# Kernel optimization log

Measured on AMD Instinct MI355X. Metric: run time of the kernel, lower is better.

Reference implementation:

```python
import jax, jax.numpy as jnp
import numpy as np

N_NODES = 50000


def gcn_conv(x, W, b, src, dst, n_nodes):
    # PyG GCNConv: h = D^{-1/2} (A + I) D^{-1/2} (x W) + b
    h = x @ W  # [N, out]
    # degree with self loops: deg[i] = in_degree(i) + 1
    deg = jax.ops.segment_sum(jnp.ones_like(dst, dtype=h.dtype), dst, num_segments=n_nodes) + 1.0
    dis = jax.lax.rsqrt(deg)  # deg >= 1 always
    norm = dis[src] * dis[dst]  # [E]
    # gather-scale-scatter over edges
    agg = jax.ops.segment_sum(h[src] * norm[:, None], dst, num_segments=n_nodes)
    # self-loop contribution: norm_ii = dis[i]^2
    agg = agg + h * (dis * dis)[:, None]
    return agg + b


def setup_inputs() -> dict:
    key = jax.random.key(0)
    k1, k2, k3, k4, k5, k6 = jax.random.split(key, 6)
    latent, hidden, out = 64, 96, 64
    x = jax.random.normal(k1, (N_NODES, latent), dtype=jnp.float32)
    edge_index = jax.random.randint(k2, (2, 800000), 0, N_NODES, dtype=jnp.int64)
    W1 = jax.random.normal(k3, (latent, hidden), dtype=jnp.float32) / np.sqrt(latent)
    b1 = jnp.zeros((hidden,), dtype=jnp.float32)
    W2 = jax.random.normal(k4, (hidden, out), dtype=jnp.float32) / np.sqrt(hidden)
    b2 = jnp.zeros((out,), dtype=jnp.float32)
    return {"x": x, "edge_index": edge_index, "W1": W1, "b1": b1, "W2": W2, "b2": b2}


def reference(x, edge_index, W1, b1, W2, b2):
    src, dst = edge_index[0], edge_index[1]
    n = x.shape[0]
    h = jax.nn.relu(gcn_conv(x, W1, b1, src, dst, n))
    out = jax.nn.sigmoid(gcn_conv(h, W2, b2, src, dst, n))
    return out
```

## Files before the change

### kernel.cpp

```cpp
#include <hip/hip_runtime.h>
#include <hip/hip_bf16.h>
#include <hip/hip_fp16.h>

constexpr int G1 = 96;
constexpr int RNODES = 12544;
constexpr int CAP = 64;

__global__ __launch_bounds__(256) void histo_kernel(const int* __restrict__ dst,
                                                    unsigned short* __restrict__ hist,
                                                    int E, int chunk, int npad2) {
    __shared__ unsigned int h32[RNODES / 2];
    int g = blockIdx.x;
    int base = blockIdx.y * RNODES;
    int e0 = g * chunk;
    int e1 = min(e0 + chunk, E);
    for (int i = threadIdx.x; i < RNODES / 2; i += 256) h32[i] = 0;
    __syncthreads();
    for (int e = e0 + threadIdx.x; e < e1; e += 256) {
        int d = dst[e] - base;
        if ((unsigned)d < (unsigned)RNODES) atomicAdd(&h32[d >> 1], 1u << ((d & 1) * 16));
    }
    __syncthreads();
    for (int i = threadIdx.x; i < RNODES; i += 256)
        hist[(size_t)g * npad2 + base + i] =
            (unsigned short)((h32[i >> 1] >> ((i & 1) * 16)) & 0xFFFFu);
}

__global__ __launch_bounds__(256) void colscan_cast_kernel(
    const unsigned short* __restrict__ hist, unsigned short* __restrict__ off16,
    int* __restrict__ cnt, float* __restrict__ dis, const float* __restrict__ x,
    __half* __restrict__ Th, int N, int npad2) {
    __shared__ float sdis[256];
    int n0 = blockIdx.x * 256;
    int d = n0 + threadIdx.x;
    float dv = 0.f;
    if (d < N) {
        int run = 0;
        for (int g = 0; g < G1; ++g) {
            off16[(size_t)g * npad2 + d] = (unsigned short)run;
            run += hist[(size_t)g * npad2 + d];
        }
        cnt[d] = run;
        dv = rsqrtf((float)run + 1.0f);
        dis[d] = dv;
    }
    sdis[threadIdx.x] = dv;
    __syncthreads();
    int total = min(256, N - n0) * 64;
    size_t base_elem = (size_t)n0 * 64;
    for (int l = threadIdx.x * 8; l < total; l += 256 * 8) {
        float dn = sdis[l >> 6];
        float4 a = *(const float4*)(x + base_elem + l);
        float4 b = *(const float4*)(x + base_elem + l + 4);
        __half2 h[4];
        h[0] = __floats2half2_rn(a.x * dn, a.y * dn);
        h[1] = __floats2half2_rn(a.z * dn, a.w * dn);
        h[2] = __floats2half2_rn(b.x * dn, b.y * dn);
        h[3] = __floats2half2_rn(b.z * dn, b.w * dn);
        *(float4*)(Th + base_elem + l) = *(float4*)h;
    }
}

__global__ __launch_bounds__(256) void fill_bucket16_kernel(
    const int* __restrict__ src, const int* __restrict__ dst,
    const unsigned short* __restrict__ off16, unsigned short* __restrict__ csr16,
    int E, int chunk, int npad2) {
    __shared__ unsigned int c16[RNODES / 2];
    int g = blockIdx.x;
    int base = blockIdx.y * RNODES;
    const unsigned int* op = (const unsigned int*)(off16 + (size_t)g * npad2 + base);
    for (int i = threadIdx.x; i < RNODES / 2; i += 256) c16[i] = op[i];
    __syncthreads();
    int e0 = g * chunk;
    int e1 = min(e0 + chunk, E);
    for (int e = e0 + threadIdx.x; e < e1; e += 256) {
        int d = dst[e] - base;
        if ((unsigned)d < (unsigned)RNODES) {
            unsigned int sh = (d & 1) * 16;
            unsigned int old = atomicAdd(&c16[d >> 1], 1u << sh);
            unsigned int rank = (old >> sh) & 0xFFFFu;
            if (rank < CAP) csr16[(size_t)(base + d) * CAP + rank] = (unsigned short)src[e];
        }
    }
}

__global__ void zero_int_kernel(int* __restrict__ p, int N) {
    int i = blockIdx.x * blockDim.x + threadIdx.x;
    if (i < N) p[i] = 0;
}
__global__ void degree_int_kernel(const int* __restrict__ dst, int* __restrict__ cnt, int E) {
    int i = blockIdx.x * blockDim.x + threadIdx.x;
    if (i < E) atomicAdd(&cnt[dst[i]], 1);
}
__global__ void dis_from_cnt_kernel(const int* __restrict__ cnt, float* __restrict__ dis, int N) {
    int i = blockIdx.x * blockDim.x + threadIdx.x;
    if (i < N) dis[i] = rsqrtf((float)cnt[i] + 1.0f);
}
__global__ __launch_bounds__(1024) void scan_kernel(const int* __restrict__ cnt,
                                                    int* __restrict__ cursor, int N) {
    constexpr int T = 1024;
    __shared__ int sums[T];
    int t = threadIdx.x;
    int ch = (N + T - 1) / T;
    int base = t * ch;
    int local = 0;
    for (int k = 0; k < ch; ++k) {
        int idx = base + k;
        if (idx < N) local += cnt[idx];
    }
    sums[t] = local;
    __syncthreads();
    for (int off = 1; off < T; off <<= 1) {
        int add = (t >= off) ? sums[t - off] : 0;
        __syncthreads();
        sums[t] += add;
        __syncthreads();
    }
    int run = sums[t] - local;
    for (int k = 0; k < ch; ++k) {
        int idx = base + k;
        if (idx < N) {
            cursor[idx] = run;
            run += cnt[idx];
        }
    }
}
__global__ void fill_atomic_kernel(const int* __restrict__ src, const int* __restrict__ dst,
                                   int* __restrict__ cursor_mut, int* __restrict__ csr_src,
                                   int E) {
    int e = blockIdx.x * blockDim.x + threadIdx.x;
    if (e >= E) return;
    int pos = atomicAdd(&cursor_mut[dst[e]], 1);
    csr_src[pos] = src[e];
}
__global__ void cast_scale_kernel(const float* __restrict__ X, const float* __restrict__ dis,
                                  __half* __restrict__ Th, int N) {
    int i = blockIdx.x * blockDim.x + threadIdx.x;
    int n = i >> 3;
    if (n >= N) return;
    int c = (i & 7) * 8;
    float dn = dis[n];
    float4 a = *(const float4*)(X + (size_t)n * 64 + c);
    float4 b = *(const float4*)(X + (size_t)n * 64 + c + 4);
    __half2 h[4];
    h[0] = __floats2half2_rn(a.x * dn, a.y * dn);
    h[1] = __floats2half2_rn(a.z * dn, a.w * dn);
    h[2] = __floats2half2_rn(b.x * dn, b.y * dn);
    h[3] = __floats2half2_rn(b.z * dn, b.w * dn);
    *(float4*)(Th + (size_t)n * 64 + c) = *(float4*)h;
}

__device__ __forceinline__ void gather_batch16(const unsigned short* __restrict__ bucket,
                                               int j0, int scnt,
                                               const __half* __restrict__ Xh, int c,
                                               float a[16]) {
    uint4 raw = *(const uint4*)(bucket + j0);
    unsigned int w[4] = {raw.x, raw.y, raw.z, raw.w};
    float4 r0[8], r1[8];
#pragma unroll
    for (int k = 0; k < 8; ++k) {
        if (k < scnt) {
            int s = (w[k >> 1] >> ((k & 1) * 16)) & 0xFFFF;
            const __half* row = Xh + (size_t)s * 64 + c;
            r0[k] = *(const float4*)(row);
            r1[k] = *(const float4*)(row + 8);
        }
    }
#pragma unroll
    for (int k = 0; k < 8; ++k) {
        if (k < scnt) {
            const __half2* h0 = (const __half2*)&r0[k];
            const __half2* h1 = (const __half2*)&r1[k];
#pragma unroll
            for (int q = 0; q < 4; ++q) {
                float2 f0 = __half22float2(h0[q]);
                float2 f1 = __half22float2(h1[q]);
                a[2 * q] += f0.x;
                a[2 * q + 1] += f0.y;
                a[8 + 2 * q] += f1.x;
                a[8 + 2 * q + 1] += f1.y;
            }
        }
    }
}

__device__ __forceinline__ void add_row16(const __half* __restrict__ row, float a[16]) {
    float4 r0 = *(const float4*)(row);
    float4 r1 = *(const float4*)(row + 8);
    const __half2* h0 = (const __half2*)&r0;
    const __half2* h1 = (const __half2*)&r1;
#pragma unroll
    for (int q = 0; q < 4; ++q) {
        float2 f0 = __half22float2(h0[q]);
        float2 f1 = __half22float2(h1[q]);
        a[2 * q] += f0.x;
        a[2 * q + 1] += f0.y;
        a[8 + 2 * q] += f1.x;
        a[8 + 2 * q + 1] += f1.y;
    }
}

template <int CAPT, typename IDX>
__global__ __launch_bounds__(256) void agg0_kernel(const int* __restrict__ cursor,
                                                   const int* __restrict__ cnt,
                                                   const IDX* __restrict__ csr,
                                                   const float* __restrict__ dis,
                                                   const __half* __restrict__ Xh,
                                                   __half* __restrict__ Yh, int N) {
    int i = blockIdx.x * 256 + threadIdx.x;
    int n = i >> 2;
    if (n >= N) return;
    int c = (i & 3) * 16;
    float a[16] = {};
    int cn = cnt[n];
    if (CAPT) {
        cn = min(cn, CAPT);
        const unsigned short* bucket = (const unsigned short*)csr + (size_t)n * CAPT;
        for (int j0 = 0; j0 < cn; j0 += 8) {
            int m = cn - j0;
            gather_batch16(bucket, j0, m < 8 ? m : 8, Xh, c, a);
        }
    } else {
        int beg = cursor[n];
        for (int j = beg; j < beg + cn; ++j)
            add_row16(Xh + (size_t)((int)csr[j]) * 64 + c, a);
    }
    add_row16(Xh + (size_t)n * 64 + c, a);
    float dn = dis[n];
    __half2 o[8];
#pragma unroll
    for (int q = 0; q < 8; ++q)
        o[q] = __floats2half2_rn(a[2 * q] * dn, a[2 * q + 1] * dn);
    __half* yp = Yh + (size_t)n * 64 + c;
    *(float4*)(yp) = ((float4*)o)[0];
    *(float4*)(yp + 8) = ((float4*)o)[1];
}

__global__ __launch_bounds__(256) void gemm12_kernel(const __half* __restrict__ Yh,
                                                     const float* __restrict__ W1,
                                                     const float* __restrict__ b1,
                                                     const float* __restrict__ W2,
                                                     const float* __restrict__ dis,
                                                     __half* __restrict__ Th2, int N) {
    constexpr int XS = 100;
    __shared__ float Xs[64 * XS];
    __shared__ float Ws[6144];
    const int n0 = blockIdx.x * 64;
    const int t = threadIdx.x;
    const int tn = t >> 4;
    const int tf = t & 15;

    for (int i = t; i < 6144 / 4; i += 256)
        ((float4*)Ws)[i] = ((const float4*)W1)[i];
    for (int i = t; i < 512; i += 256) {
        int row = i >> 3;
        int c8 = (i & 7) * 8;
        float4 raw = make_float4(0.f, 0.f, 0.f, 0.f);
        if (n0 + row < N) raw = *(const float4*)(Yh + (size_t)(n0 + row) * 64 + c8);
        const __half2* hp = (const __half2*)&raw;
        float* p = Xs + row * XS + c8;
#pragma unroll
        for (int q = 0; q < 4; ++q) {
            float2 f = __half22float2(hp[q]);
            p[2 * q] = f.x;
            p[2 * q + 1] = f.y;
        }
    }
    float breg[6];
#pragma unroll
    for (int j = 0; j < 6; ++j) breg[j] = b1[tf * 6 + j];
    __syncthreads();

    float h[4][6] = {};
    for (int k0 = 0; k0 < 64; k0 += 4) {
        float4 xv[4];
#pragma unroll
        for (int i = 0; i < 4; ++i) xv[i] = *(const float4*)(Xs + (tn * 4 + i) * XS + k0);
        float wv[4][6];
#pragma unroll
        for (int j4 = 0; j4 < 4; ++j4)
#pragma unroll
            for (int j = 0; j < 3; ++j) {
                float2 w2 = *(const float2*)(Ws + (k0 + j4) * 96 + tf * 6 + 2 * j);
                wv[j4][2 * j] = w2.x;
                wv[j4][2 * j + 1] = w2.y;
            }
#pragma unroll
        for (int i = 0; i < 4; ++i) {
            const float xk[4] = {xv[i].x, xv[i].y, xv[i].z, xv[i].w};
#pragma unroll
            for (int j4 = 0; j4 < 4; ++j4)
#pragma unroll
                for (int j = 0; j < 6; ++j) h[i][j] += xk[j4] * wv[j4][j];
        }
    }
#pragma unroll
    for (int i = 0; i < 4; ++i)
#pragma unroll
        for (int j = 0; j < 6; ++j) h[i][j] = fmaxf(h[i][j] + breg[j], 0.f);
    __syncthreads();

#pragma unroll
    for (int i = 0; i < 4; ++i)
#pragma unroll
        for (int j = 0; j < 6; ++j) Xs[(tn * 4 + i) * XS + tf * 6 + j] = h[i][j];
    for (int i = t; i < 6144 / 4; i += 256)
        ((float4*)Ws)[i] = ((const float4*)W2)[i];
    __syncthreads();

    float acc[4][4] = {};
    for (int k0 = 0; k0 < 96; k0 += 4) {
        float4 xv[4];
#pragma unroll
        for (int i = 0; i < 4; ++i) xv[i] = *(const float4*)(Xs + (tn * 4 + i) * XS + k0);
        float wv[4][4];
#pragma unroll
        for (int j4 = 0; j4 < 4; ++j4)
#pragma unroll
            for (int j = 0; j < 2; ++j) {
                float2 w2 = *(const float2*)(Ws + (k0 + j4) * 64 + tf * 4 + 2 * j);
                wv[j4][2 * j] = w2.x;
                wv[j4][2 * j + 1] = w2.y;
            }
#pragma unroll
        for (int i = 0; i < 4; ++i) {
            const float xk[4] = {xv[i].x, xv[i].y, xv[i].z, xv[i].w};
#pragma unroll
            for (int j4 = 0; j4 < 4; ++j4)
#pragma unroll
                for (int j = 0; j < 4; ++j) acc[i][j] += xk[j4] * wv[j4][j];
        }
    }
#pragma unroll
    for (int i = 0; i < 4; ++i) {
        int n = n0 + tn * 4 + i;
        if (n < N) {
            float dn = dis[n];
            __half* op = Th2 + (size_t)n * 64 + tf * 4;
            *(__half2*)(op) = __floats2half2_rn(acc[i][0] * dn, acc[i][1] * dn);
            *(__half2*)(op + 2) = __floats2half2_rn(acc[i][2] * dn, acc[i][3] * dn);
        }
    }
}

template <int CAPT, typename IDX>
__global__ __launch_bounds__(256) void agg1_kernel(const int* __restrict__ cursor,
                                                   const int* __restrict__ cnt,
                                                   const IDX* __restrict__ csr,
                                                   const float* __restrict__ dis,
                                                   const __half* __restrict__ Xh,
                                                   const float* __restrict__ b,
                                                   float* __restrict__ out, int N) {
    int i = blockIdx.x * 256 + threadIdx.x;
    int n = i >> 2;
    if (n >= N) return;
    int c = (i & 3) * 16;
    float a[16] = {};
    int cn = cnt[n];
    if (CAPT) {
        cn = min(cn, CAPT);
        const unsigned short* bucket = (const unsigned short*)csr + (size_t)n * CAPT;
        for (int j0 = 0; j0 < cn; j0 += 8) {
            int m = cn - j0;
            gather_batch16(bucket, j0, m < 8 ? m : 8, Xh, c, a);
        }
    } else {
        int beg = cursor[n];
        for (int j = beg; j < beg + cn; ++j)
            add_row16(Xh + (size_t)((int)csr[j]) * 64 + c, a);
    }
    add_row16(Xh + (size_t)n * 64 + c, a);
    float dn = dis[n];
    float r[16];
#pragma unroll
    for (int q = 0; q < 16; ++q) r[q] = 1.f / (1.f + expf(-(a[q] * dn + b[c + q])));
    float* op = out + (size_t)n * 64 + c;
    *(float4*)(op) = make_float4(r[0], r[1], r[2], r[3]);
    *(float4*)(op + 4) = make_float4(r[4], r[5], r[6], r[7]);
    *(float4*)(op + 8) = make_float4(r[8], r[9], r[10], r[11]);
    *(float4*)(op + 12) = make_float4(r[12], r[13], r[14], r[15]);
}

extern "C" void kernel_launch(void* const* d_in, const int* in_sizes, int n_in,
                              void* d_out, int out_size, void* d_ws, size_t ws_size,
                              hipStream_t stream) {
    const float* x  = (const float*)d_in[0];
    const int*   ei = (const int*)d_in[1];
    const float* W1 = (const float*)d_in[2];
    const float* b1 = (const float*)d_in[3];
    const float* W2 = (const float*)d_in[4];
    const float* b2 = (const float*)d_in[5];

    constexpr int LAT = 64;
    const int E = in_sizes[1] / 2;
    const int N = in_sizes[0] / LAT;
    const int* src = ei;
    const int* dst = ei + E;

    const int B = 256;
    auto blocks = [](long total, int b) { return (int)((total + b - 1) / b); };

    const int ranges = (N + RNODES - 1) / RNODES;
    const int npad2 = ranges * RNODES;
    const int chunk = (E + G1 - 1) / G1;

    long nmax = (npad2 > N) ? npad2 : N;
    size_t Na = (size_t)((nmax + 1023) / 1024) * 1024;
    size_t Epad = (size_t)((E + 3) / 4) * 4;
    size_t csrBytes = (size_t)Na * CAP * 2;
    if (csrBytes < Epad * 4) csrBytes = Epad * 4;
    csrBytes = (csrBytes + 15) / 16 * 16;

    int* cnt      = (int*)d_ws;
    int* cursor   = cnt + Na;
    int* cursmut  = cursor + Na;
    float* dis    = (float*)(cursmut + Na);
    char* csr_raw = (char*)(dis + Na);
    unsigned short* csr16 = (unsigned short*)csr_raw;
    int*            csr32 = (int*)csr_raw;
    unsigned short* hist  = (unsigned short*)(csr_raw + csrBytes);
    unsigned short* off16 = hist + (size_t)G1 * npad2;
    __half* Th  = (__half*)(off16 + (size_t)G1 * npad2);
    __half* Th2 = Th + Na * 64;
    __half* Yh  = Th2 + Na * 64;

    size_t need = (char*)(Yh + Na * 64) - (char*)d_ws;
    bool fast = (ws_size >= need) && (chunk < 65536) && (ranges <= 16) && (N <= 65535);

    if (fast) {
        dim3 g2(G1, ranges);
        histo_kernel<<<g2, 256, 0, stream>>>(dst, hist, E, chunk, npad2);
        colscan_cast_kernel<<<blocks(N, 256), 256, 0, stream>>>(hist, off16, cnt, dis, x, Th,
                                                                N, npad2);
        fill_bucket16_kernel<<<g2, 256, 0, stream>>>(src, dst, off16, csr16, E, chunk, npad2);
        agg0_kernel<CAP, unsigned short>
            <<<blocks((long)N * 4, B), B, 0, stream>>>(nullptr, cnt, csr16, dis, Th, Yh, N);
        gemm12_kernel<<<blocks(N, 64), 256, 0, stream>>>(Yh, W1, b1, W2, dis, Th2, N);
        agg1_kernel<CAP, unsigned short>
            <<<blocks((long)N * 4, B), B, 0, stream>>>(nullptr, cnt, csr16, dis, Th2, b2,
                                                       (float*)d_out, N);
    } else {
        zero_int_kernel<<<blocks(N, B), B, 0, stream>>>(cnt, N);
        degree_int_kernel<<<blocks(E, B), B, 0, stream>>>(dst, cnt, E);
        dis_from_cnt_kernel<<<blocks(N, B), B, 0, stream>>>(cnt, dis, N);
        scan_kernel<<<1, 1024, 0, stream>>>(cnt, cursor, N);
        hipMemcpyAsync(cursmut, cursor, (size_t)N * sizeof(int), hipMemcpyDeviceToDevice, stream);
        fill_atomic_kernel<<<blocks(E, B), B, 0, stream>>>(src, dst, cursmut, csr32, E);
        cast_scale_kernel<<<blocks((long)N * 8, B), B, 0, stream>>>(x, dis, Th, N);
        agg0_kernel<0, int>
            <<<blocks((long)N * 4, B), B, 0, stream>>>(cursor, cnt, csr32, dis, Th, Yh, N);
        gemm12_kernel<<<blocks(N, 64), 256, 0, stream>>>(Yh, W1, b1, W2, dis, Th2, N);
        agg1_kernel<0, int>
            <<<blocks((long)N * 4, B), B, 0, stream>>>(cursor, cnt, csr32, dis, Th2, b2,
                                                       (float*)d_out, N);
    }
}
```

Before: 183.0 us.

## Fuse first-layer aggregation into the two-layer GEMM kernel

Adds a kernel that gathers each node's neighbor rows, scales them by the degree normalisation, and writes them straight into shared memory. The same block then runs both dense layers, so the fp16 intermediate Yh is never written or read back and one launch is removed. The column scan now preloads all 96 histogram entries into registers before scanning, and the final sigmoid outputs use nontemporal stores. The fused kernel holds about 50KB of shared memory and a large register set, which can lower occupancy for the latency-bound gather phase.

```diff
diff --git a/kernel.cpp b/kernel.cpp
--- a/kernel.cpp
+++ b/kernel.cpp
@@ -1,6 +1,8 @@
 #include <hip/hip_runtime.h>
 #include <hip/hip_bf16.h>
 #include <hip/hip_fp16.h>
+
+typedef float nt_f4 __attribute__((ext_vector_type(4)));
 
 constexpr int G1 = 96;
 constexpr int RNODES = 12544;
@@ -35,10 +37,14 @@
     int d = n0 + threadIdx.x;
     float dv = 0.f;
     if (d < N) {
+        unsigned int hv[G1];
+#pragma unroll
+        for (int g = 0; g < G1; ++g) hv[g] = hist[(size_t)g * npad2 + d];
         int run = 0;
+#pragma unroll
         for (int g = 0; g < G1; ++g) {
             off16[(size_t)g * npad2 + d] = (unsigned short)run;
-            run += hist[(size_t)g * npad2 + d];
+            run += (int)hv[g];
         }
         cnt[d] = run;
         dv = rsqrtf((float)run + 1.0f);
@@ -234,6 +240,131 @@
     __half* yp = Yh + (size_t)n * 64 + c;
     *(float4*)(yp) = ((float4*)o)[0];
     *(float4*)(yp + 8) = ((float4*)o)[1];
+}
+
+template <int CAPT, typename IDX>
+__global__ __launch_bounds__(256) void agg0_gemm_kernel(
+    const int* __restrict__ cursor, const int* __restrict__ cnt,
+    const IDX* __restrict__ csr, const float* __restrict__ dis,
+    const __half* __restrict__ Xh, const float* __restrict__ W1,
+    const float* __restrict__ b1, const float* __restrict__ W2,
+    __half* __restrict__ Th2, int N) {
+    constexpr int XS = 100;
+    __shared__ float Xs[64 * XS];
+    __shared__ float Ws[6144];
+    const int t = threadIdx.x;
+    const int n0 = blockIdx.x * 64;
+    const int tn = t >> 4;
+    const int tf = t & 15;
+
+    for (int i = t; i < 6144 / 4; i += 256)
+        ((float4*)Ws)[i] = ((const float4*)W1)[i];
+
+    {
+        int n = n0 + (t >> 2);
+        int c = (t & 3) * 16;
+        float a[16] = {};
+        float dn = 0.f;
+        if (n < N) {
+            int cn = cnt[n];
+            if (CAPT) {
+                cn = min(cn, CAPT);
+                const unsigned short* bucket = (const unsigned short*)csr + (size_t)n * CAPT;
+                for (int j0 = 0; j0 < cn; j0 += 8) {
+                    int m = cn - j0;
+                    gather_batch16(bucket, j0, m < 8 ? m : 8, Xh, c, a);
+                }
+            } else {
+                int beg = cursor[n];
+                for (int j = beg; j < beg + cn; ++j)
+                    add_row16(Xh + (size_t)((int)csr[j]) * 64 + c, a);
+            }
+            add_row16(Xh + (size_t)n * 64 + c, a);
+            dn = dis[n];
+        }
+        float* xp = Xs + (size_t)(t >> 2) * XS + c;
+#pragma unroll
+        for (int q = 0; q < 4; ++q) {
+            float4 v = make_float4(a[4 * q] * dn, a[4 * q + 1] * dn, a[4 * q + 2] * dn,
+                                   a[4 * q + 3] * dn);
+            *(float4*)(xp + 4 * q) = v;
+        }
+    }
+    float breg[6];
+#pragma unroll
+    for (int j = 0; j < 6; ++j) breg[j] = b1[tf * 6 + j];
+    __syncthreads();
+
+    float h[4][6] = {};
+    for (int k0 = 0; k0 < 64; k0 += 4) {
+        float4 xv[4];
+#pragma unroll
+        for (int i = 0; i < 4; ++i) xv[i] = *(const float4*)(Xs + (tn * 4 + i) * XS + k0);
+        float wv[4][6];
+#pragma unroll
+        for (int j4 = 0; j4 < 4; ++j4)
+#pragma unroll
+            for (int j = 0; j < 3; ++j) {
+                float2 w2 = *(const float2*)(Ws + (k0 + j4) * 96 + tf * 6 + 2 * j);
+                wv[j4][2 * j] = w2.x;
+                wv[j4][2 * j + 1] = w2.y;
+            }
+#pragma unroll
+        for (int i = 0; i < 4; ++i) {
+            const float xk[4] = {xv[i].x, xv[i].y, xv[i].z, xv[i].w};
+#pragma unroll
+            for (int j4 = 0; j4 < 4; ++j4)
+#pragma unroll
+                for (int j = 0; j < 6; ++j) h[i][j] += xk[j4] * wv[j4][j];
+        }
+    }
+#pragma unroll
+    for (int i = 0; i < 4; ++i)
+#pragma unroll
+        for (int j = 0; j < 6; ++j) h[i][j] = fmaxf(h[i][j] + breg[j], 0.f);
+    __syncthreads();
+
+#pragma unroll
+    for (int i = 0; i < 4; ++i)
+#pragma unroll
+        for (int j = 0; j < 6; ++j) Xs[(tn * 4 + i) * XS + tf * 6 + j] = h[i][j];
+    for (int i = t; i < 6144 / 4; i += 256)
+        ((float4*)Ws)[i] = ((const float4*)W2)[i];
+    __syncthreads();
+
+    float acc[4][4] = {};
+    for (int k0 = 0; k0 < 96; k0 += 4) {
+        float4 xv[4];
+#pragma unroll
+        for (int i = 0; i < 4; ++i) xv[i] = *(const float4*)(Xs + (tn * 4 + i) * XS + k0);
+        float wv[4][4];
+#pragma unroll
+        for (int j4 = 0; j4 < 4; ++j4)
+#pragma unroll
+            for (int j = 0; j < 2; ++j) {
+                float2 w2 = *(const float2*)(Ws + (k0 + j4) * 64 + tf * 4 + 2 * j);
+                wv[j4][2 * j] = w2.x;
+                wv[j4][2 * j + 1] = w2.y;
+            }
+#pragma unroll
+        for (int i = 0; i < 4; ++i) {
+            const float xk[4] = {xv[i].x, xv[i].y, xv[i].z, xv[i].w};
+#pragma unroll
+            for (int j4 = 0; j4 < 4; ++j4)
+#pragma unroll
+                for (int j = 0; j < 4; ++j) acc[i][j] += xk[j4] * wv[j4][j];
+        }
+    }
+#pragma unroll
+    for (int i = 0; i < 4; ++i) {
+        int n = n0 + tn * 4 + i;
+        if (n < N) {
+            float dn = dis[n];
+            __half* op = Th2 + (size_t)n * 64 + tf * 4;
+            *(__half2*)(op) = __floats2half2_rn(acc[i][0] * dn, acc[i][1] * dn);
+            *(__half2*)(op + 2) = __floats2half2_rn(acc[i][2] * dn, acc[i][3] * dn);
+        }
+    }
 }
 
 __global__ __launch_bounds__(256) void gemm12_kernel(const __half* __restrict__ Yh,
@@ -375,10 +506,10 @@
 #pragma unroll
     for (int q = 0; q < 16; ++q) r[q] = 1.f / (1.f + expf(-(a[q] * dn + b[c + q])));
     float* op = out + (size_t)n * 64 + c;
-    *(float4*)(op) = make_float4(r[0], r[1], r[2], r[3]);
-    *(float4*)(op + 4) = make_float4(r[4], r[5], r[6], r[7]);
-    *(float4*)(op + 8) = make_float4(r[8], r[9], r[10], r[11]);
-    *(float4*)(op + 12) = make_float4(r[12], r[13], r[14], r[15]);
+    __builtin_nontemporal_store((nt_f4){r[0], r[1], r[2], r[3]}, (nt_f4*)(op));
+    __builtin_nontemporal_store((nt_f4){r[4], r[5], r[6], r[7]}, (nt_f4*)(op + 4));
+    __builtin_nontemporal_store((nt_f4){r[8], r[9], r[10], r[11]}, (nt_f4*)(op + 8));
+    __builtin_nontemporal_store((nt_f4){r[12], r[13], r[14], r[15]}, (nt_f4*)(op + 12));
 }
 
 extern "C" void kernel_launch(void* const* d_in, const int* in_sizes, int n_in,
@@ -433,9 +564,9 @@
         colscan_cast_kernel<<<blocks(N, 256), 256, 0, stream>>>(hist, off16, cnt, dis, x, Th,
                                                                 N, npad2);
         fill_bucket16_kernel<<<g2, 256, 0, stream>>>(src, dst, off16, csr16, E, chunk, npad2);
-        agg0_kernel<CAP, unsigned short>
-            <<<blocks((long)N * 4, B), B, 0, stream>>>(nullptr, cnt, csr16, dis, Th, Yh, N);
-        gemm12_kernel<<<blocks(N, 64), 256, 0, stream>>>(Yh, W1, b1, W2, dis, Th2, N);
+        agg0_gemm_kernel<CAP, unsigned short>
+            <<<blocks(N, 64), 256, 0, stream>>>(nullptr, cnt, csr16, dis, Th, W1, b1, W2,
+                                                Th2, N);
         agg1_kernel<CAP, unsigned short>
             <<<blocks((long)N * 4, B), B, 0, stream>>>(nullptr, cnt, csr16, dis, Th2, b2,
                                                        (float*)d_out, N);
```

Result: no change. 181.8 us (-0.6%).
